# Performance work log

Hardware: AMD Instinct MI355X
Metric: run time of the kernel (lower is better)

The kernel has to match this reference:

```python
import jax, jax.numpy as jnp
import numpy as np

HIDDEN = 512

def setup_inputs() -> dict:
    key = jax.random.key(0)
    ks = jax.random.split(key, 9)
    B, S, H = 64, 2048, HIDDEN
    scale = 1.0 / np.sqrt(H)
    return {
        "decoder_state": jax.random.normal(ks[0], (B, H), dtype=jnp.float32),
        "encoder_outputs": jax.random.normal(ks[1], (B, S, 2 * H), dtype=jnp.float32),
        "encoder_mask": jax.random.randint(ks[2], (B, S), 0, 2, dtype=jnp.int32),
        "coverage": jax.random.uniform(ks[3], (B, S), dtype=jnp.float32),
        "W_h": jax.random.normal(ks[4], (2 * H, H), dtype=jnp.float32) * scale,
        "W_s": jax.random.normal(ks[5], (H, H), dtype=jnp.float32) * scale,
        "b_s": jax.random.normal(ks[6], (H,), dtype=jnp.float32) * scale,
        "W_c": jax.random.normal(ks[7], (1, H), dtype=jnp.float32) * scale,
        "v": jax.random.normal(ks[8], (H, 1), dtype=jnp.float32) * scale,
    }


def reference(decoder_state, encoder_outputs, encoder_mask, coverage, W_h, W_s, b_s, W_c, v):
    # encoder_features: (B, S, H)
    enc_feat = jnp.einsum('bsk,kh->bsh', encoder_outputs, W_h)
    # decoder_features: (B, 1, H), broadcast over S
    dec_feat = (decoder_state @ W_s + b_s)[:, None, :]
    # coverage features: (B, S, 1) @ (1, H) -> (B, S, H) == outer product
    cov_feat = coverage[:, :, None] * W_c[0][None, None, :]
    att = jnp.tanh(enc_feat + dec_feat + cov_feat)
    e = jnp.einsum('bsh,h->bs', att, v[:, 0])  # (B, S)
    e = jnp.where(encoder_mask == 0, jnp.float32(-10000.0), e)
    attention_dist = jax.nn.softmax(e, axis=1)  # (B, S)
    # context: (B, 1, S) bmm (B, S, 2H) -> (B, 2H)
    context_vector = jnp.einsum('bs,bsk->bk', attention_dist, encoder_outputs)
    new_coverage = coverage + attention_dist
    return (context_vector, attention_dist, new_coverage)
```

## Files before the change

### kernel.cpp

```cpp
#include <hip/hip_runtime.h>
#include <hip/hip_bf16.h>

#define BATCH 64
#define SEQ   2048
#define HDIM  512
#define K2H   1024
#define MROWS (BATCH * SEQ)

typedef __bf16 bf16_t;
using bf16x8  = __attribute__((ext_vector_type(8))) __bf16;
using bf16x4  = __attribute__((ext_vector_type(4))) __bf16;
using floatx4 = __attribute__((ext_vector_type(4))) float;

__global__ void dec_feat_kernel(const float* __restrict__ dec,
                                const float* __restrict__ Ws,
                                const float* __restrict__ bs,
                                float* __restrict__ out) {
    const int b = blockIdx.x;
    const int h = threadIdx.x;
    const float* dr = dec + b * HDIM;
    float acc = bs[h];
#pragma unroll 8
    for (int k = 0; k < HDIM; ++k)
        acc += dr[k] * Ws[k * HDIM + h];
    out[b * HDIM + h] = acc;
}

__global__ void pack_wh_kernel(const float* __restrict__ Wh,
                               bf16_t* __restrict__ Wt) {
    const int id = blockIdx.x * 256 + threadIdx.x;
    const int k = id >> 9;
    const int n = id & 511;
    const int kk = k >> 5;
    const int q  = (k >> 3) & 3;
    const int j  = k & 7;
    const int nt = n >> 4;
    const int r  = n & 15;
    const int off = (((kk * 32 + nt) * 64) + (q * 16 + r)) * 8 + j;
    Wt[off] = (bf16_t)Wh[id];
}

__launch_bounds__(512)
__global__ void escore_kernel(const float* __restrict__ enc,
                              const bf16_t* __restrict__ Wt,
                              const float* __restrict__ decf,
                              const float* __restrict__ cov,
                              const float* __restrict__ Wc,
                              const float* __restrict__ v,
                              float* __restrict__ e_out) {
    __shared__ bf16_t Alds[64][72];
    __shared__ float red[8][64];

    const int tid  = threadIdx.x;
    const int wave = tid >> 6;
    const int lane = tid & 63;
    const int r = lane & 15, q = lane >> 4;
    const int m0 = blockIdx.x * 64;

    floatx4 acc[4][4];
#pragma unroll
    for (int a = 0; a < 4; ++a)
#pragma unroll
        for (int c = 0; c < 4; ++c) acc[a][c] = (floatx4){0.f, 0.f, 0.f, 0.f};

    const int row0 = tid >> 4;
    const int col4 = tid & 15;

    for (int kk2 = 0; kk2 < 16; ++kk2) {
        float4 f0 = *(const float4*)&enc[(size_t)(m0 + row0) * K2H + kk2 * 64 + col4 * 4];
        float4 f1 = *(const float4*)&enc[(size_t)(m0 + row0 + 32) * K2H + kk2 * 64 + col4 * 4];
        __syncthreads();
        {
            bf16x4 b0, b1;
            b0.x = (bf16_t)f0.x; b0.y = (bf16_t)f0.y; b0.z = (bf16_t)f0.z; b0.w = (bf16_t)f0.w;
            b1.x = (bf16_t)f1.x; b1.y = (bf16_t)f1.y; b1.z = (bf16_t)f1.z; b1.w = (bf16_t)f1.w;
            *(bf16x4*)&Alds[row0][col4 * 4]      = b0;
            *(bf16x4*)&Alds[row0 + 32][col4 * 4] = b1;
        }
        __syncthreads();
#pragma unroll
        for (int ks = 0; ks < 2; ++ks) {
            const int kkg = kk2 * 2 + ks;
            bf16x8 bfr[4];
#pragma unroll
            for (int ntl = 0; ntl < 4; ++ntl) {
                const int ntg = wave * 4 + ntl;
                bfr[ntl] = *(const bf16x8*)&Wt[(((size_t)(kkg * 32 + ntg)) * 64 + lane) * 8];
            }
#pragma unroll
            for (int mt = 0; mt < 4; ++mt) {
                bf16x8 afr = *(const bf16x8*)&Alds[mt * 16 + r][ks * 32 + q * 8];
#pragma unroll
                for (int ntl = 0; ntl < 4; ++ntl)
                    acc[mt][ntl] = __builtin_amdgcn_mfma_f32_16x16x32_bf16(
                        afr, bfr[ntl], acc[mt][ntl], 0, 0, 0);
            }
        }
    }

    const int b     = m0 >> 11;
    const int sbase = m0 & 2047;
    float dval[4], wcv[4], vv[4];
#pragma unroll
    for (int ntl = 0; ntl < 4; ++ntl) {
        const int n = wave * 64 + ntl * 16 + r;
        dval[ntl] = decf[b * HDIM + n];
        wcv[ntl]  = Wc[n];
        vv[ntl]   = v[n];
    }
#pragma unroll
    for (int mt = 0; mt < 4; ++mt) {
#pragma unroll
        for (int i = 0; i < 4; ++i) {
            const int mloc = mt * 16 + q * 4 + i;
            const float cm = cov[b * SEQ + sbase + mloc];
            float p = 0.f;
#pragma unroll
            for (int ntl = 0; ntl < 4; ++ntl) {
                float x = acc[mt][ntl][i] + dval[ntl] + cm * wcv[ntl];
                x = fminf(fmaxf(x, -15.f), 15.f);
                float z = __expf(2.f * x);
                p += (1.f - 2.f / (z + 1.f)) * vv[ntl];
            }
#pragma unroll
            for (int off = 1; off < 16; off <<= 1)
                p += __shfl_xor(p, off, 64);
            if (r == 0) red[wave][mloc] = p;
        }
    }
    __syncthreads();
    if (tid < 64) {
        float s = 0.f;
#pragma unroll
        for (int w = 0; w < 8; ++w) s += red[w][tid];
        e_out[(size_t)m0 + tid] = s;
    }
}

__global__ void softmax_kernel(float* ed,
                               const int* __restrict__ mask,
                               const float* __restrict__ cov,
                               float* __restrict__ ncov) {
    const int b = blockIdx.x, tid = threadIdx.x;
    __shared__ float wred[4];
    float ev[8];
    float mx = -1e30f;
#pragma unroll
    for (int i = 0; i < 8; ++i) {
        const int s = tid + i * 256;
        float e = ed[b * SEQ + s];
        e = (mask[b * SEQ + s] == 0) ? -10000.f : e;
        ev[i] = e;
        mx = fmaxf(mx, e);
    }
#pragma unroll
    for (int off = 32; off; off >>= 1) mx = fmaxf(mx, __shfl_xor(mx, off, 64));
    if ((tid & 63) == 0) wred[tid >> 6] = mx;
    __syncthreads();
    mx = fmaxf(fmaxf(wred[0], wred[1]), fmaxf(wred[2], wred[3]));
    __syncthreads();
    float sum = 0.f;
#pragma unroll
    for (int i = 0; i < 8; ++i) { ev[i] = __expf(ev[i] - mx); sum += ev[i]; }
#pragma unroll
    for (int off = 32; off; off >>= 1) sum += __shfl_xor(sum, off, 64);
    if ((tid & 63) == 0) wred[tid >> 6] = sum;
    __syncthreads();
    sum = wred[0] + wred[1] + wred[2] + wred[3];
    const float inv = 1.f / sum;
#pragma unroll
    for (int i = 0; i < 8; ++i) {
        const int s = tid + i * 256;
        const float d = ev[i] * inv;
        ed[b * SEQ + s]   = d;
        ncov[b * SEQ + s] = cov[b * SEQ + s] + d;
    }
}

__global__ void context_kernel(const float* __restrict__ enc,
                               const float* __restrict__ dist,
                               float* __restrict__ ctx) {
    const int b = blockIdx.x, sc = blockIdx.y, tid = threadIdx.x;
    __shared__ float wl[256];
    wl[tid] = dist[b * SEQ + sc * 256 + tid];
    __syncthreads();
    float4 a = {0.f, 0.f, 0.f, 0.f};
    const float* base = enc + (size_t)(b * SEQ + sc * 256) * K2H + tid * 4;
#pragma unroll 4
    for (int s = 0; s < 256; ++s) {
        const float w = wl[s];
        float4 xv = *(const float4*)(base + (size_t)s * K2H);
        a.x += w * xv.x; a.y += w * xv.y; a.z += w * xv.z; a.w += w * xv.w;
    }
    float* o = ctx + b * K2H + tid * 4;
    atomicAdd(o + 0, a.x);
    atomicAdd(o + 1, a.y);
    atomicAdd(o + 2, a.z);
    atomicAdd(o + 3, a.w);
}

extern "C" void kernel_launch(void* const* d_in, const int* in_sizes, int n_in,
                              void* d_out, int out_size, void* d_ws, size_t ws_size,
                              hipStream_t stream) {
    const float* dec  = (const float*)d_in[0];
    const float* enc  = (const float*)d_in[1];
    const int*   mask = (const int*)d_in[2];
    const float* cov  = (const float*)d_in[3];
    const float* Wh   = (const float*)d_in[4];
    const float* Ws   = (const float*)d_in[5];
    const float* bs   = (const float*)d_in[6];
    const float* Wc   = (const float*)d_in[7];
    const float* v    = (const float*)d_in[8];

    float* out  = (float*)d_out;
    float* ctx  = out;
    float* dist = out + BATCH * K2H;
    float* ncov = dist + BATCH * SEQ;

    bf16_t* Wt   = (bf16_t*)d_ws;
    float*  decf = (float*)((char*)d_ws + (1 << 20));

    hipMemsetAsync(ctx, 0, BATCH * K2H * sizeof(float), stream);
    pack_wh_kernel<<<2048, 256, 0, stream>>>(Wh, Wt);
    dec_feat_kernel<<<BATCH, 512, 0, stream>>>(dec, Ws, bs, decf);
    escore_kernel<<<MROWS / 64, 512, 0, stream>>>(enc, Wt, decf, cov, Wc, v, dist);
    softmax_kernel<<<BATCH, 256, 0, stream>>>(dist, mask, cov, ncov);
    context_kernel<<<dim3(BATCH, 8), 256, 0, stream>>>(enc, dist, ctx);
}
```

Measured before the change: 916.9 us.

## Double-buffer escore LDS tiles and reuse bf16 encoder copy for context

```diff
diff --git a/kernel.cpp b/kernel.cpp
--- a/kernel.cpp
+++ b/kernel.cpp
@@ -29,26 +29,30 @@
 __global__ void pack_wh_kernel(const float* __restrict__ Wh,
                                bf16_t* __restrict__ Wt) {
     const int id = blockIdx.x * 256 + threadIdx.x;
-    const int k = id >> 9;
-    const int n = id & 511;
-    const int kk = k >> 5;
-    const int q  = (k >> 3) & 3;
-    const int j  = k & 7;
-    const int nt = n >> 4;
-    const int r  = n & 15;
-    const int off = (((kk * 32 + nt) * 64) + (q * 16 + r)) * 8 + j;
-    Wt[off] = (bf16_t)Wh[id];
-}
-
-__launch_bounds__(512)
+    const int r  = id & 15;
+    const int nt = (id >> 4) & 31;
+    const int q  = (id >> 9) & 3;
+    const int kk = id >> 11;
+    const int lane  = q * 16 + r;
+    const int kbase = kk * 32 + q * 8;
+    const int n     = nt * 16 + r;
+    bf16x8 w;
+#pragma unroll
+    for (int j = 0; j < 8; ++j)
+        w[j] = (bf16_t)Wh[(kbase + j) * HDIM + n];
+    *(bf16x8*)&Wt[(((kk * 32 + nt) * 64) + lane) * 8] = w;
+}
+
+__launch_bounds__(512, 4)
 __global__ void escore_kernel(const float* __restrict__ enc,
                               const bf16_t* __restrict__ Wt,
                               const float* __restrict__ decf,
                               const float* __restrict__ cov,
                               const float* __restrict__ Wc,
                               const float* __restrict__ v,
-                              float* __restrict__ e_out) {
-    __shared__ bf16_t Alds[64][72];
+                              float* __restrict__ e_out,
+                              bf16_t* __restrict__ encb) {
+    __shared__ bf16_t Alds[2][64][72];
     __shared__ float red[8][64];
 
     const int tid  = threadIdx.x;
@@ -65,19 +69,31 @@
 
     const int row0 = tid >> 4;
     const int col4 = tid & 15;
+    const float* g0 = &enc[(size_t)(m0 + row0) * K2H + col4 * 4];
+    const float* g1 = &enc[(size_t)(m0 + row0 + 32) * K2H + col4 * 4];
+    bf16_t* e0 = &encb[(size_t)(m0 + row0) * K2H + col4 * 4];
+    bf16_t* e1 = &encb[(size_t)(m0 + row0 + 32) * K2H + col4 * 4];
+
+    {
+        float4 f0 = *(const float4*)g0;
+        float4 f1 = *(const float4*)g1;
+        bf16x4 b0, b1;
+        b0.x = (bf16_t)f0.x; b0.y = (bf16_t)f0.y; b0.z = (bf16_t)f0.z; b0.w = (bf16_t)f0.w;
+        b1.x = (bf16_t)f1.x; b1.y = (bf16_t)f1.y; b1.z = (bf16_t)f1.z; b1.w = (bf16_t)f1.w;
+        *(bf16x4*)&Alds[0][row0][col4 * 4]      = b0;
+        *(bf16x4*)&Alds[0][row0 + 32][col4 * 4] = b1;
+        *(bf16x4*)e0 = b0;
+        *(bf16x4*)e1 = b1;
+    }
+    __syncthreads();
 
     for (int kk2 = 0; kk2 < 16; ++kk2) {
-        float4 f0 = *(const float4*)&enc[(size_t)(m0 + row0) * K2H + kk2 * 64 + col4 * 4];
-        float4 f1 = *(const float4*)&enc[(size_t)(m0 + row0 + 32) * K2H + kk2 * 64 + col4 * 4];
-        __syncthreads();
-        {
-            bf16x4 b0, b1;
-            b0.x = (bf16_t)f0.x; b0.y = (bf16_t)f0.y; b0.z = (bf16_t)f0.z; b0.w = (bf16_t)f0.w;
-            b1.x = (bf16_t)f1.x; b1.y = (bf16_t)f1.y; b1.z = (bf16_t)f1.z; b1.w = (bf16_t)f1.w;
-            *(bf16x4*)&Alds[row0][col4 * 4]      = b0;
-            *(bf16x4*)&Alds[row0 + 32][col4 * 4] = b1;
-        }
-        __syncthreads();
+        const int cur = kk2 & 1;
+        float4 n0, n1;
+        if (kk2 < 15) {
+            n0 = *(const float4*)(g0 + (kk2 + 1) * 64);
+            n1 = *(const float4*)(g1 + (kk2 + 1) * 64);
+        }
 #pragma unroll
         for (int ks = 0; ks < 2; ++ks) {
             const int kkg = kk2 * 2 + ks;
@@ -89,13 +105,23 @@
             }
 #pragma unroll
             for (int mt = 0; mt < 4; ++mt) {
-                bf16x8 afr = *(const bf16x8*)&Alds[mt * 16 + r][ks * 32 + q * 8];
+                bf16x8 afr = *(const bf16x8*)&Alds[cur][mt * 16 + r][ks * 32 + q * 8];
 #pragma unroll
                 for (int ntl = 0; ntl < 4; ++ntl)
                     acc[mt][ntl] = __builtin_amdgcn_mfma_f32_16x16x32_bf16(
                         afr, bfr[ntl], acc[mt][ntl], 0, 0, 0);
             }
         }
+        if (kk2 < 15) {
+            bf16x4 b0, b1;
+            b0.x = (bf16_t)n0.x; b0.y = (bf16_t)n0.y; b0.z = (bf16_t)n0.z; b0.w = (bf16_t)n0.w;
+            b1.x = (bf16_t)n1.x; b1.y = (bf16_t)n1.y; b1.z = (bf16_t)n1.z; b1.w = (bf16_t)n1.w;
+            *(bf16x4*)&Alds[cur ^ 1][row0][col4 * 4]      = b0;
+            *(bf16x4*)&Alds[cur ^ 1][row0 + 32][col4 * 4] = b1;
+            *(bf16x4*)(e0 + (kk2 + 1) * 64) = b0;
+            *(bf16x4*)(e1 + (kk2 + 1) * 64) = b1;
+        }
+        __syncthreads();
     }
 
     const int b     = m0 >> 11;
@@ -177,20 +203,21 @@
     }
 }
 
-__global__ void context_kernel(const float* __restrict__ enc,
+__global__ void context_kernel(const bf16_t* __restrict__ encb,
                                const float* __restrict__ dist,
                                float* __restrict__ ctx) {
     const int b = blockIdx.x, sc = blockIdx.y, tid = threadIdx.x;
-    __shared__ float wl[256];
-    wl[tid] = dist[b * SEQ + sc * 256 + tid];
+    __shared__ float wl[128];
+    if (tid < 128) wl[tid] = dist[b * SEQ + sc * 128 + tid];
     __syncthreads();
     float4 a = {0.f, 0.f, 0.f, 0.f};
-    const float* base = enc + (size_t)(b * SEQ + sc * 256) * K2H + tid * 4;
+    const bf16_t* base = encb + (size_t)(b * SEQ + sc * 128) * K2H + tid * 4;
 #pragma unroll 4
-    for (int s = 0; s < 256; ++s) {
+    for (int s = 0; s < 128; ++s) {
         const float w = wl[s];
-        float4 xv = *(const float4*)(base + (size_t)s * K2H);
-        a.x += w * xv.x; a.y += w * xv.y; a.z += w * xv.z; a.w += w * xv.w;
+        bf16x4 xv = *(const bf16x4*)(base + (size_t)s * K2H);
+        a.x += w * (float)xv[0]; a.y += w * (float)xv[1];
+        a.z += w * (float)xv[2]; a.w += w * (float)xv[3];
     }
     float* o = ctx + b * K2H + tid * 4;
     atomicAdd(o + 0, a.x);
@@ -219,11 +246,12 @@
 
     bf16_t* Wt   = (bf16_t*)d_ws;
     float*  decf = (float*)((char*)d_ws + (1 << 20));
+    bf16_t* encb = (bf16_t*)((char*)d_ws + (2 << 20));
 
     hipMemsetAsync(ctx, 0, BATCH * K2H * sizeof(float), stream);
-    pack_wh_kernel<<<2048, 256, 0, stream>>>(Wh, Wt);
+    pack_wh_kernel<<<256, 256, 0, stream>>>(Wh, Wt);
     dec_feat_kernel<<<BATCH, 512, 0, stream>>>(dec, Ws, bs, decf);
-    escore_kernel<<<MROWS / 64, 512, 0, stream>>>(enc, Wt, decf, cov, Wc, v, dist);
+    escore_kernel<<<MROWS / 64, 512, 0, stream>>>(enc, Wt, decf, cov, Wc, v, dist, encb);
     softmax_kernel<<<BATCH, 256, 0, stream>>>(dist, mask, cov, ncov);
-    context_kernel<<<dim3(BATCH, 8), 256, 0, stream>>>(enc, dist, ctx);
-}
+    context_kernel<<<dim3(BATCH, 16), 256, 0, stream>>>(encb, dist, ctx);
+}
```

Result: slower. 944.9 us (+3.1%).
